# Kernel tuning notes

Measured on AMD Instinct MI355X. Metric: run time of the kernel, lower is better.

The kernel has to match this reference:

```python
import jax, jax.numpy as jnp
import numpy as np

NUM_HEADS = 16

def setup_inputs() -> dict:
    key = jax.random.key(0)
    ks = jax.random.split(key, 7)
    n_node, n_graph, E = 512, 8, 1024
    H = NUM_HEADS
    inp = {
        "query": jax.random.normal(ks[0], (n_node, n_graph, E), jnp.float32),
        "attn_bias": jax.random.normal(ks[1], (n_graph * H, n_node, n_node), jnp.float32),
        "graph_attn_weight": jax.random.normal(ks[2], (n_graph * H, n_node, n_node), jnp.float32),
        "in_w": jax.random.normal(ks[3], (3 * E, E), jnp.float32) * (E ** -0.5),
        "in_b": jnp.zeros((3 * E,), jnp.float32),
        "out_w": jax.random.normal(ks[4], (E, E), jnp.float32) * (E ** -0.5),
        "out_b": jnp.zeros((E,), jnp.float32),
    }
    return inp

def reference(query, attn_bias, graph_attn_weight, in_w, in_b, out_w, out_b):
    n_node, n_graph, E = query.shape
    H = NUM_HEADS
    hd = E // H
    scaling = hd ** -0.5
    # fused QKV projection (torch Linear: x @ W.T + b)
    qkv = query @ in_w.T + in_b                      # [n, g, 3E]
    q, k, v = jnp.split(qkv, 3, axis=-1)             # each [n, g, E]
    def to_heads(x):
        # [n, g, E] -> [g*H, n, hd]
        return x.reshape(n_node, n_graph * H, hd).transpose(1, 0, 2)
    q = to_heads(q) * scaling
    k = to_heads(k)
    v = to_heads(v)
    attn_weights = jnp.einsum('bnd,bmd->bnm', q, k) + attn_bias  # [g*H, n, n]
    attn_probs = jnp.tanh(graph_attn_weight) * jax.nn.softmax(attn_weights, axis=-1)
    attn = jnp.einsum('bnm,bmd->bnd', attn_probs, v)             # [g*H, n, hd]
    attn = attn.transpose(1, 0, 2).reshape(n_node, n_graph, E)
    return attn @ out_w.T + out_b
```

## Files before the change

kernel.cpp:

```cpp
#include <hip/hip_runtime.h>
#include <hip/hip_bf16.h>
#include <cstdint>

#define N_NODE 512
#define N_GRAPH 8
#define EDIM 1024
#define NHEADS 16
#define HD 64
#define GH 128
#define MROWS 4096

typedef short bf16x8 __attribute__((ext_vector_type(8)));
typedef float f32x4  __attribute__((ext_vector_type(4)));

__device__ __forceinline__ short f2bs(float f) {
    union { __hip_bfloat16 h; short s; } u; u.h = __float2bfloat16(f); return u.s;
}
__device__ __forceinline__ float bs2f(short s) {
    union { unsigned u; float f; } v; v.u = ((unsigned)(unsigned short)s) << 16; return v.f;
}
__device__ __forceinline__ float fast_tanh(float x) {
    const float e = __expf(2.f * x);
    return 1.f - __fdividef(2.f, 1.f + e);
}

__device__ __forceinline__ void direct_lds16(const short* g, short* l) {
    __builtin_amdgcn_global_load_lds(
        (const __attribute__((address_space(1))) unsigned int*)(uintptr_t)g,
        (__attribute__((address_space(3))) unsigned int*)(unsigned)(uintptr_t)l,
        16, 0, 0);
}

__global__ __launch_bounds__(256)
void cvt_bf16(const float* __restrict__ in, short* __restrict__ out, int n8)
{
    const int i = blockIdx.x * 256 + threadIdx.x;
    if (i >= n8) return;
    const float4 f0 = *reinterpret_cast<const float4*>(in + (size_t)i * 8);
    const float4 f1 = *reinterpret_cast<const float4*>(in + (size_t)i * 8 + 4);
    bf16x8 h;
    h[0] = f2bs(f0.x); h[1] = f2bs(f0.y); h[2] = f2bs(f0.z); h[3] = f2bs(f0.w);
    h[4] = f2bs(f1.x); h[5] = f2bs(f1.y); h[6] = f2bs(f1.z); h[7] = f2bs(f1.w);
    *reinterpret_cast<bf16x8*>(out + (size_t)i * 8) = h;
}

template<int MODE>
__global__ __launch_bounds__(256)
void gemm_bf16(const short* __restrict__ A, const short* __restrict__ B,
               const float* __restrict__ bias, float* __restrict__ Cout,
               __hip_bfloat16* __restrict__ Cq,
               __hip_bfloat16* __restrict__ Ck,
               __hip_bfloat16* __restrict__ Cv,
               int M, int N, int K)
{
    __shared__ short As[128 * 32];
    __shared__ short Bs[128 * 32];

    const int nwg  = gridDim.x * gridDim.y;
    const int flat = blockIdx.y * gridDim.x + blockIdx.x;
    const int q8   = nwg >> 3;
    const int swz  = (flat & 7) * q8 + (flat >> 3);
    const int bx   = swz % gridDim.x;
    const int by   = swz / gridDim.x;

    const int tid  = threadIdx.x;
    const int m0   = by * 128;
    const int n0   = bx * 128;
    const int lane = tid & 63;
    const int w    = tid >> 6;
    const int l16  = lane & 15;
    const int quad = lane >> 4;
    const int wm   = w & 1;
    const int wn   = w >> 1;
    const int lrow = lane >> 2;
    const int lcol = (lane & 3) << 3;

    const short* ga = A + (size_t)(m0 + w * 16 + lrow) * K + lcol;
    const short* gb = B + (size_t)(n0 + w * 16 + lrow) * K + lcol;
    short* lA = &As[w * 512];
    short* lB = &Bs[w * 512];

    f32x4 acc[4][4];
    #pragma unroll
    for (int mt = 0; mt < 4; mt++)
        #pragma unroll
        for (int nt = 0; nt < 4; nt++)
            acc[mt][nt] = (f32x4){0.f, 0.f, 0.f, 0.f};

    for (int k0 = 0; k0 < K; k0 += 32) {
        direct_lds16(ga + k0, lA);
        direct_lds16(ga + (size_t)64 * K + k0, lA + 2048);
        direct_lds16(gb + k0, lB);
        direct_lds16(gb + (size_t)64 * K + k0, lB + 2048);
        __syncthreads();

        bf16x8 af[4], bfr[4];
        #pragma unroll
        for (int mt = 0; mt < 4; mt++)
            af[mt] = *reinterpret_cast<const bf16x8*>(
                &As[(wm * 64 + mt * 16 + l16) * 32 + quad * 8]);
        #pragma unroll
        for (int nt = 0; nt < 4; nt++)
            bfr[nt] = *reinterpret_cast<const bf16x8*>(
                &Bs[(wn * 64 + nt * 16 + l16) * 32 + quad * 8]);
        #pragma unroll
        for (int mt = 0; mt < 4; mt++)
            #pragma unroll
            for (int nt = 0; nt < 4; nt++)
                acc[mt][nt] = __builtin_amdgcn_mfma_f32_16x16x32_bf16(
                    af[mt], bfr[nt], acc[mt][nt], 0, 0, 0);
        __syncthreads();
    }

    #pragma unroll
    for (int nt = 0; nt < 4; nt++) {
        const int c = n0 + wn * 64 + nt * 16 + l16;
        const float bv = bias[c];
        #pragma unroll
        for (int mt = 0; mt < 4; mt++) {
            #pragma unroll
            for (int rr = 0; rr < 4; rr++) {
                const int r = m0 + wm * 64 + mt * 16 + quad * 4 + rr;
                const float v = acc[mt][nt][rr] + bv;
                if (MODE == 0) {
                    Cout[(size_t)r * N + c] = v;
                } else {
                    const int qsel = c >> 10;
                    const int e = c & 1023;
                    const int head = e >> 6;
                    const int d = e & 63;
                    const int node = r >> 3;
                    const int graph = r & 7;
                    const int b = graph * NHEADS + head;
                    const size_t idx = ((size_t)b * N_NODE + node) * HD + d;
                    if (qsel == 0)      Cq[idx] = __float2bfloat16(v * 0.125f);
                    else if (qsel == 1) Ck[idx] = __float2bfloat16(v);
                    else                Cv[idx] = __float2bfloat16(v);
                }
            }
        }
    }
}

__global__ __launch_bounds__(256)
void transpose_v(const __hip_bfloat16* __restrict__ V,
                 __hip_bfloat16* __restrict__ Vt)
{
    __shared__ short T[64][80];
    const int b = blockIdx.y;
    const int jt = blockIdx.x;
    const int t = threadIdx.x;

    #pragma unroll
    for (int it = 0; it < 2; it++) {
        const int idx = t + it * 256;
        const int j_loc = idx >> 3;
        const int ch = idx & 7;
        bf16x8 v = *reinterpret_cast<const bf16x8*>(
            V + ((size_t)b * N_NODE + jt * 64 + j_loc) * HD + ch * 8);
        *reinterpret_cast<bf16x8*>(&T[j_loc][ch * 8]) = v;
    }
    __syncthreads();
    #pragma unroll
    for (int it = 0; it < 2; it++) {
        const int idx = t + it * 256;
        const int d_loc = idx >> 3;
        const int ch = idx & 7;
        bf16x8 o;
        #pragma unroll
        for (int x = 0; x < 8; x++) o[x] = T[ch * 8 + x][d_loc];
        *reinterpret_cast<bf16x8*>(
            Vt + ((size_t)b * HD + d_loc) * N_NODE + jt * 64 + ch * 8) = o;
    }
}

#define PBS 512

__global__ __launch_bounds__(256, 4)
void attn_mfma(const __hip_bfloat16* __restrict__ Qh,
               const __hip_bfloat16* __restrict__ Kh,
               const __hip_bfloat16* __restrict__ Vt,
               const float* __restrict__ bias,
               const float* __restrict__ gaw,
               __hip_bfloat16* __restrict__ A2)
{
    __shared__ __align__(16) short Pb[16 * PBS];
    __shared__ __align__(16) float mpart[16][4];
    __shared__ __align__(16) float spart[16][4];

    const int b    = blockIdx.y;
    const int i0   = blockIdx.x * 16;
    const int tid  = threadIdx.x;
    const int lane = tid & 63;
    const int w    = tid >> 6;
    const int quad = lane >> 4;
    const int l16  = lane & 15;
    const int row_l = quad * 4;

    f32x4 sreg[8];

    {
        const __hip_bfloat16* Qb =
            Qh + ((size_t)b * N_NODE + i0 + l16) * HD + quad * 8;
        const bf16x8 qa0 = *reinterpret_cast<const bf16x8*>(Qb);
        const bf16x8 qa1 = *reinterpret_cast<const bf16x8*>(Qb + 32);
        const float* bp0 = bias + ((size_t)b * N_NODE + i0 + row_l) * N_NODE + l16;
        float mx[4] = {-1e30f, -1e30f, -1e30f, -1e30f};

        #pragma unroll
        for (int t = 0; t < 8; t++) {
            const int jt = w + 4 * t;
            const __hip_bfloat16* Kb =
                Kh + ((size_t)b * N_NODE + jt * 16 + l16) * HD + quad * 8;
            const bf16x8 k0 = *reinterpret_cast<const bf16x8*>(Kb);
            const bf16x8 k1 = *reinterpret_cast<const bf16x8*>(Kb + 32);
            f32x4 acc = {0.f, 0.f, 0.f, 0.f};
            acc = __builtin_amdgcn_mfma_f32_16x16x32_bf16(qa0, k0, acc, 0, 0, 0);
            acc = __builtin_amdgcn_mfma_f32_16x16x32_bf16(qa1, k1, acc, 0, 0, 0);
            const float* bp = bp0 + jt * 16;
            #pragma unroll
            for (int r = 0; r < 4; r++) {
                acc[r] += bp[(size_t)r * N_NODE];
                mx[r] = fmaxf(mx[r], acc[r]);
            }
            sreg[t] = acc;
        }
        #pragma unroll
        for (int r = 0; r < 4; r++) {
            float m = mx[r];
            m = fmaxf(m, __shfl_xor(m, 1));
            m = fmaxf(m, __shfl_xor(m, 2));
            m = fmaxf(m, __shfl_xor(m, 4));
            m = fmaxf(m, __shfl_xor(m, 8));
            if (l16 == 0) mpart[row_l + r][w] = m;
        }
    }
    __syncthreads();

    {
        float mrow[4];
        #pragma unroll
        for (int r = 0; r < 4; r++) {
            const float4 mp = *reinterpret_cast<const float4*>(mpart[row_l + r]);
            mrow[r] = fmaxf(fmaxf(mp.x, mp.y), fmaxf(mp.z, mp.w));
        }
        float sum[4] = {0.f, 0.f, 0.f, 0.f};
        const float* gp0 = gaw + ((size_t)b * N_NODE + i0 + row_l) * N_NODE + l16;

        #pragma unroll
        for (int t = 0; t < 8; t++) {
            const int jt = w + 4 * t;
            const int colb = (jt * 16 + l16) * 2;
            const float* gp = gp0 + jt * 16;
            #pragma unroll
            for (int r = 0; r < 4; r++) {
                const float e = __expf(sreg[t][r] - mrow[r]);
                sum[r] += e;
                const float g = gp[(size_t)r * N_NODE];
                const float p = fast_tanh(g) * e;
                const int row = row_l + r;
                const int byte = row * (PBS * 2) + (colb ^ ((row & 7) << 4));
                *reinterpret_cast<short*>(reinterpret_cast<char*>(Pb) + byte) = f2bs(p);
            }
        }
        #pragma unroll
        for (int r = 0; r < 4; r++) {
            float s = sum[r];
            s += __shfl_xor(s, 1);
            s += __shfl_xor(s, 2);
            s += __shfl_xor(s, 4);
            s += __shfl_xor(s, 8);
            if (l16 == 0) spart[row_l + r][w] = s;
        }
    }
    __syncthreads();

    {
        const __hip_bfloat16* Vb =
            Vt + ((size_t)b * HD + w * 16 + l16) * N_NODE + quad * 8;
        f32x4 acc = {0.f, 0.f, 0.f, 0.f};
        #pragma unroll
        for (int j32 = 0; j32 < 16; j32++) {
            const int byte = l16 * (PBS * 2)
                           + ((j32 * 64 + quad * 16) ^ ((l16 & 7) << 4));
            const bf16x8 af = *reinterpret_cast<const bf16x8*>(
                reinterpret_cast<const char*>(Pb) + byte);
            const bf16x8 bfr = *reinterpret_cast<const bf16x8*>(Vb + j32 * 32);
            acc = __builtin_amdgcn_mfma_f32_16x16x32_bf16(af, bfr, acc, 0, 0, 0);
        }
        const int node0 = i0 + quad * 4;
        __hip_bfloat16* op = A2 + (size_t)node0 * (N_GRAPH * EDIM)
                           + (b >> 4) * EDIM + (b & 15) * HD + w * 16 + l16;
        #pragma unroll
        for (int r = 0; r < 4; r++) {
            const float4 sp = *reinterpret_cast<const float4*>(spart[quad * 4 + r]);
            const float rs = 1.f / (sp.x + sp.y + sp.z + sp.w);
            op[(size_t)r * (N_GRAPH * EDIM)] = __float2bfloat16(acc[r] * rs);
        }
    }
}

extern "C" void kernel_launch(void* const* d_in, const int* in_sizes, int n_in,
                              void* d_out, int out_size, void* d_ws, size_t ws_size,
                              hipStream_t stream) {
    const float* query     = (const float*)d_in[0];
    const float* attn_bias = (const float*)d_in[1];
    const float* gaw       = (const float*)d_in[2];
    const float* in_w      = (const float*)d_in[3];
    const float* in_b      = (const float*)d_in[4];
    const float* out_w     = (const float*)d_in[5];
    const float* out_b     = (const float*)d_in[6];
    float* out = (float*)d_out;

    short* wsp = (short*)d_ws;
    const size_t hsz = (size_t)GH * N_NODE * HD;
    short* Q   = wsp;
    short* K   = wsp + hsz;
    short* V   = wsp + 2 * hsz;
    short* Vt  = wsp + 3 * hsz;
    short* A2  = V;
    short* qb  = Vt;
    short* wbi = wsp + 4 * hsz;
    short* wbo = wbi + (size_t)3 * EDIM * EDIM;

    cvt_bf16<<<dim3(MROWS * EDIM / 2048), 256, 0, stream>>>(query, qb, MROWS * EDIM / 8);
    cvt_bf16<<<dim3(3 * EDIM * EDIM / 2048), 256, 0, stream>>>(in_w, wbi, 3 * EDIM * EDIM / 8);
    cvt_bf16<<<dim3(EDIM * EDIM / 2048), 256, 0, stream>>>(out_w, wbo, EDIM * EDIM / 8);

    gemm_bf16<1><<<dim3(24, 32), 256, 0, stream>>>(
        qb, wbi, in_b, nullptr,
        (__hip_bfloat16*)Q, (__hip_bfloat16*)K, (__hip_bfloat16*)V,
        MROWS, 3 * EDIM, EDIM);

    transpose_v<<<dim3(8, GH), 256, 0, stream>>>(
        (const __hip_bfloat16*)V, (__hip_bfloat16*)Vt);

    attn_mfma<<<dim3(N_NODE / 16, GH), 256, 0, stream>>>(
        (const __hip_bfloat16*)Q, (const __hip_bfloat16*)K,
        (const __hip_bfloat16*)Vt, attn_bias, gaw, (__hip_bfloat16*)A2);

    gemm_bf16<0><<<dim3(8, 32), 256, 0, stream>>>(
        (const short*)A2, wbo, out_b, out,
        nullptr, nullptr, nullptr, MROWS, EDIM, EDIM);
}
```

Baseline: 426.7 us.

## Pipeline GEMM loads with triple buffering and restructure attention for vectorized loads

The GEMM now uses a three-stage LDS ring with direct global-to-LDS loads issued one tile ahead and explicit vmcnt waits, replacing the two-barrier-per-iteration loop. It gains a BN template so the output projection uses 64-wide tiles and a larger grid. The attention kernel swaps the MFMA operand order so each lane owns one row, which allows float4 loads of bias and graph weights. It also prefetches K and V fragments into registers, swizzles the block order, and lowers launch bounds to 3 waves per SIMD. The trade is higher register and LDS pressure, and less occupancy, in return for overlapping memory with compute and coalescing the reads.

```diff
diff --git a/kernel.cpp b/kernel.cpp
--- a/kernel.cpp
+++ b/kernel.cpp
@@ -15,9 +15,6 @@
 
 __device__ __forceinline__ short f2bs(float f) {
     union { __hip_bfloat16 h; short s; } u; u.h = __float2bfloat16(f); return u.s;
-}
-__device__ __forceinline__ float bs2f(short s) {
-    union { unsigned u; float f; } v; v.u = ((unsigned)(unsigned short)s) << 16; return v.f;
 }
 __device__ __forceinline__ float fast_tanh(float x) {
     const float e = __expf(2.f * x);
@@ -44,7 +41,7 @@
     *reinterpret_cast<bf16x8*>(out + (size_t)i * 8) = h;
 }
 
-template<int MODE>
+template<int MODE, int BN>
 __global__ __launch_bounds__(256)
 void gemm_bf16(const short* __restrict__ A, const short* __restrict__ B,
                const float* __restrict__ bias, float* __restrict__ Cout,
@@ -53,8 +50,8 @@
                __hip_bfloat16* __restrict__ Cv,
                int M, int N, int K)
 {
-    __shared__ short As[128 * 32];
-    __shared__ short Bs[128 * 32];
+    __shared__ short As[3][128 * 32];
+    __shared__ short Bs[3][BN * 32];
 
     const int nwg  = gridDim.x * gridDim.y;
     const int flat = blockIdx.y * gridDim.x + blockIdx.x;
@@ -65,7 +62,7 @@
 
     const int tid  = threadIdx.x;
     const int m0   = by * 128;
-    const int n0   = bx * 128;
+    const int n0   = bx * BN;
     const int lane = tid & 63;
     const int w    = tid >> 6;
     const int l16  = lane & 15;
@@ -77,44 +74,65 @@
 
     const short* ga = A + (size_t)(m0 + w * 16 + lrow) * K + lcol;
     const short* gb = B + (size_t)(n0 + w * 16 + lrow) * K + lcol;
-    short* lA = &As[w * 512];
-    short* lB = &Bs[w * 512];
-
-    f32x4 acc[4][4];
+
+    constexpr int NTC = BN / 32;
+
+    f32x4 acc[4][NTC];
     #pragma unroll
     for (int mt = 0; mt < 4; mt++)
         #pragma unroll
-        for (int nt = 0; nt < 4; nt++)
+        for (int nt = 0; nt < NTC; nt++)
             acc[mt][nt] = (f32x4){0.f, 0.f, 0.f, 0.f};
 
-    for (int k0 = 0; k0 < K; k0 += 32) {
-        direct_lds16(ga + k0, lA);
-        direct_lds16(ga + (size_t)64 * K + k0, lA + 2048);
-        direct_lds16(gb + k0, lB);
-        direct_lds16(gb + (size_t)64 * K + k0, lB + 2048);
-        __syncthreads();
-
-        bf16x8 af[4], bfr[4];
+    auto STAGE = [&](int kk, int buf) {
+        short* lA = &As[buf][w * 512];
+        direct_lds16(ga + kk, lA);
+        direct_lds16(ga + (size_t)64 * K + kk, lA + 2048);
+        short* lB = &Bs[buf][w * 512];
+        direct_lds16(gb + kk, lB);
+        if constexpr (BN == 128)
+            direct_lds16(gb + (size_t)64 * K + kk, lB + 2048);
+    };
+
+    const int NT = K >> 5;
+    STAGE(0, 0);
+    int cur = 0, nxt = 1;
+    for (int t = 0; t < NT; ++t) {
+        if (t + 1 < NT) {
+            STAGE((t + 1) << 5, nxt);
+            if constexpr (BN == 128)
+                asm volatile("s_waitcnt vmcnt(4)" ::: "memory");
+            else
+                asm volatile("s_waitcnt vmcnt(3)" ::: "memory");
+        } else {
+            asm volatile("s_waitcnt vmcnt(0)" ::: "memory");
+        }
+        __builtin_amdgcn_s_barrier();
+        __builtin_amdgcn_sched_barrier(0);
+
+        bf16x8 af[4], bfr[NTC];
         #pragma unroll
         for (int mt = 0; mt < 4; mt++)
             af[mt] = *reinterpret_cast<const bf16x8*>(
-                &As[(wm * 64 + mt * 16 + l16) * 32 + quad * 8]);
-        #pragma unroll
-        for (int nt = 0; nt < 4; nt++)
+                &As[cur][(wm * 64 + mt * 16 + l16) * 32 + quad * 8]);
+        #pragma unroll
+        for (int nt = 0; nt < NTC; nt++)
             bfr[nt] = *reinterpret_cast<const bf16x8*>(
-                &Bs[(wn * 64 + nt * 16 + l16) * 32 + quad * 8]);
+                &Bs[cur][(wn * (BN / 2) + nt * 16 + l16) * 32 + quad * 8]);
         #pragma unroll
         for (int mt = 0; mt < 4; mt++)
             #pragma unroll
-            for (int nt = 0; nt < 4; nt++)
+            for (int nt = 0; nt < NTC; nt++)
                 acc[mt][nt] = __builtin_amdgcn_mfma_f32_16x16x32_bf16(
                     af[mt], bfr[nt], acc[mt][nt], 0, 0, 0);
-        __syncthreads();
-    }
-
-    #pragma unroll
-    for (int nt = 0; nt < 4; nt++) {
-        const int c = n0 + wn * 64 + nt * 16 + l16;
+
+        cur = (cur == 2) ? 0 : cur + 1;
+        nxt = (nxt == 2) ? 0 : nxt + 1;
+    }
+
+    #pragma unroll
+    for (int nt = 0; nt < NTC; nt++) {
+        const int c = n0 + wn * (BN / 2) + nt * 16 + l16;
         const float bv = bias[c];
         #pragma unroll
         for (int mt = 0; mt < 4; mt++) {
@@ -174,9 +192,7 @@
     }
 }
 
-#define PBS 512
-
-__global__ __launch_bounds__(256, 4)
+__global__ __launch_bounds__(256, 3)
 void attn_mfma(const __hip_bfloat16* __restrict__ Qh,
                const __hip_bfloat16* __restrict__ Kh,
                const __hip_bfloat16* __restrict__ Vt,
@@ -184,109 +200,109 @@
                const float* __restrict__ gaw,
                __hip_bfloat16* __restrict__ A2)
 {
-    __shared__ __align__(16) short Pb[16 * PBS];
+    __shared__ __align__(16) short Pb[16 * 512];
     __shared__ __align__(16) float mpart[16][4];
     __shared__ __align__(16) float spart[16][4];
 
-    const int b    = blockIdx.y;
-    const int i0   = blockIdx.x * 16;
+    const int flat = blockIdx.y * gridDim.x + blockIdx.x;
+    const int swz  = (flat & 7) * 512 + (flat >> 3);
+    const int b    = swz >> 5;
+    const int i0   = (swz & 31) * 16;
+
     const int tid  = threadIdx.x;
     const int lane = tid & 63;
     const int w    = tid >> 6;
     const int quad = lane >> 4;
     const int l16  = lane & 15;
-    const int row_l = quad * 4;
+
+    const bf16x8* Qb = reinterpret_cast<const bf16x8*>(
+        Qh + ((size_t)b * N_NODE + i0 + l16) * HD + quad * 8);
+    const bf16x8 qa0 = Qb[0];
+    const bf16x8 qa1 = Qb[4];
+
+    bf16x8 kf[8][2];
+    #pragma unroll
+    for (int t = 0; t < 8; ++t) {
+        const int jt = w + 4 * t;
+        const bf16x8* Kb = reinterpret_cast<const bf16x8*>(
+            Kh + ((size_t)b * N_NODE + jt * 16 + l16) * HD + quad * 8);
+        kf[t][0] = Kb[0];
+        kf[t][1] = Kb[4];
+    }
+    const float* bp0 = bias + ((size_t)b * N_NODE + i0 + l16) * N_NODE
+                     + w * 16 + quad * 4;
+    f32x4 breg[8];
+    #pragma unroll
+    for (int t = 0; t < 8; ++t)
+        breg[t] = *reinterpret_cast<const f32x4*>(bp0 + t * 64);
 
     f32x4 sreg[8];
+    float mx = -1e30f;
+    #pragma unroll
+    for (int t = 0; t < 8; ++t) {
+        f32x4 acc = {0.f, 0.f, 0.f, 0.f};
+        acc = __builtin_amdgcn_mfma_f32_16x16x32_bf16(kf[t][0], qa0, acc, 0, 0, 0);
+        acc = __builtin_amdgcn_mfma_f32_16x16x32_bf16(kf[t][1], qa1, acc, 0, 0, 0);
+        acc += breg[t];
+        sreg[t] = acc;
+        mx = fmaxf(mx, fmaxf(fmaxf(acc[0], acc[1]), fmaxf(acc[2], acc[3])));
+    }
+
+    const float* gp0 = gaw + ((size_t)b * N_NODE + i0 + l16) * N_NODE
+                     + w * 16 + quad * 4;
+    f32x4 greg[8];
+    #pragma unroll
+    for (int t = 0; t < 8; ++t)
+        greg[t] = *reinterpret_cast<const f32x4*>(gp0 + t * 64);
+
+    mx = fmaxf(mx, __shfl_xor(mx, 16));
+    mx = fmaxf(mx, __shfl_xor(mx, 32));
+    if (lane < 16) mpart[l16][w] = mx;
+    __syncthreads();
+
+    const float4 mp4 = *reinterpret_cast<const float4*>(mpart[l16]);
+    const float m = fmaxf(fmaxf(mp4.x, mp4.y), fmaxf(mp4.z, mp4.w));
+
+    const bf16x8* Vb = reinterpret_cast<const bf16x8*>(
+        Vt + ((size_t)b * HD + w * 16 + l16) * N_NODE + quad * 8);
+    bf16x8 vf[16];
+    #pragma unroll
+    for (int j32 = 0; j32 < 16; ++j32)
+        vf[j32] = Vb[j32 * 4];
+
+    float sum = 0.f;
+    #pragma unroll
+    for (int t = 0; t < 8; ++t) {
+        const int jt = w + 4 * t;
+        short4 p4;
+        {
+            const float e0 = __expf(sreg[t][0] - m);
+            const float e1 = __expf(sreg[t][1] - m);
+            const float e2 = __expf(sreg[t][2] - m);
+            const float e3 = __expf(sreg[t][3] - m);
+            sum += (e0 + e1) + (e2 + e3);
+            p4.x = f2bs(fast_tanh(greg[t][0]) * e0);
+            p4.y = f2bs(fast_tanh(greg[t][1]) * e1);
+            p4.z = f2bs(fast_tanh(greg[t][2]) * e2);
+            p4.w = f2bs(fast_tanh(greg[t][3]) * e3);
+        }
+        const int byte = l16 * 1024 + ((jt * 32 + quad * 8) ^ ((l16 & 7) << 4));
+        *reinterpret_cast<short4*>(reinterpret_cast<char*>(Pb) + byte) = p4;
+    }
+    sum += __shfl_xor(sum, 16);
+    sum += __shfl_xor(sum, 32);
+    if (lane < 16) spart[l16][w] = sum;
+    __syncthreads();
 
     {
-        const __hip_bfloat16* Qb =
-            Qh + ((size_t)b * N_NODE + i0 + l16) * HD + quad * 8;
-        const bf16x8 qa0 = *reinterpret_cast<const bf16x8*>(Qb);
-        const bf16x8 qa1 = *reinterpret_cast<const bf16x8*>(Qb + 32);
-        const float* bp0 = bias + ((size_t)b * N_NODE + i0 + row_l) * N_NODE + l16;
-        float mx[4] = {-1e30f, -1e30f, -1e30f, -1e30f};
-
-        #pragma unroll
-        for (int t = 0; t < 8; t++) {
-            const int jt = w + 4 * t;
-            const __hip_bfloat16* Kb =
-                Kh + ((size_t)b * N_NODE + jt * 16 + l16) * HD + quad * 8;
-            const bf16x8 k0 = *reinterpret_cast<const bf16x8*>(Kb);
-            const bf16x8 k1 = *reinterpret_cast<const bf16x8*>(Kb + 32);
-            f32x4 acc = {0.f, 0.f, 0.f, 0.f};
-            acc = __builtin_amdgcn_mfma_f32_16x16x32_bf16(qa0, k0, acc, 0, 0, 0);
-            acc = __builtin_amdgcn_mfma_f32_16x16x32_bf16(qa1, k1, acc, 0, 0, 0);
-            const float* bp = bp0 + jt * 16;
-            #pragma unroll
-            for (int r = 0; r < 4; r++) {
-                acc[r] += bp[(size_t)r * N_NODE];
-                mx[r] = fmaxf(mx[r], acc[r]);
-            }
-            sreg[t] = acc;
-        }
-        #pragma unroll
-        for (int r = 0; r < 4; r++) {
-            float m = mx[r];
-            m = fmaxf(m, __shfl_xor(m, 1));
-            m = fmaxf(m, __shfl_xor(m, 2));
-            m = fmaxf(m, __shfl_xor(m, 4));
-            m = fmaxf(m, __shfl_xor(m, 8));
-            if (l16 == 0) mpart[row_l + r][w] = m;
-        }
-    }
-    __syncthreads();
-
-    {
-        float mrow[4];
-        #pragma unroll
-        for (int r = 0; r < 4; r++) {
-            const float4 mp = *reinterpret_cast<const float4*>(mpart[row_l + r]);
-            mrow[r] = fmaxf(fmaxf(mp.x, mp.y), fmaxf(mp.z, mp.w));
-        }
-        float sum[4] = {0.f, 0.f, 0.f, 0.f};
-        const float* gp0 = gaw + ((size_t)b * N_NODE + i0 + row_l) * N_NODE + l16;
-
-        #pragma unroll
-        for (int t = 0; t < 8; t++) {
-            const int jt = w + 4 * t;
-            const int colb = (jt * 16 + l16) * 2;
-            const float* gp = gp0 + jt * 16;
-            #pragma unroll
-            for (int r = 0; r < 4; r++) {
-                const float e = __expf(sreg[t][r] - mrow[r]);
-                sum[r] += e;
-                const float g = gp[(size_t)r * N_NODE];
-                const float p = fast_tanh(g) * e;
-                const int row = row_l + r;
-                const int byte = row * (PBS * 2) + (colb ^ ((row & 7) << 4));
-                *reinterpret_cast<short*>(reinterpret_cast<char*>(Pb) + byte) = f2bs(p);
-            }
-        }
-        #pragma unroll
-        for (int r = 0; r < 4; r++) {
-            float s = sum[r];
-            s += __shfl_xor(s, 1);
-            s += __shfl_xor(s, 2);
-            s += __shfl_xor(s, 4);
-            s += __shfl_xor(s, 8);
-            if (l16 == 0) spart[row_l + r][w] = s;
-        }
-    }
-    __syncthreads();
-
-    {
-        const __hip_bfloat16* Vb =
-            Vt + ((size_t)b * HD + w * 16 + l16) * N_NODE + quad * 8;
         f32x4 acc = {0.f, 0.f, 0.f, 0.f};
         #pragma unroll
-        for (int j32 = 0; j32 < 16; j32++) {
-            const int byte = l16 * (PBS * 2)
+        for (int j32 = 0; j32 < 16; ++j32) {
+            const int byte = l16 * 1024
                            + ((j32 * 64 + quad * 16) ^ ((l16 & 7) << 4));
             const bf16x8 af = *reinterpret_cast<const bf16x8*>(
                 reinterpret_cast<const char*>(Pb) + byte);
-            const bf16x8 bfr = *reinterpret_cast<const bf16x8*>(Vb + j32 * 32);
-            acc = __builtin_amdgcn_mfma_f32_16x16x32_bf16(af, bfr, acc, 0, 0, 0);
+            acc = __builtin_amdgcn_mfma_f32_16x16x32_bf16(af, vf[j32], acc, 0, 0, 0);
         }
         const int node0 = i0 + quad * 4;
         __hip_bfloat16* op = A2 + (size_t)node0 * (N_GRAPH * EDIM)
@@ -327,7 +343,7 @@
     cvt_bf16<<<dim3(3 * EDIM * EDIM / 2048), 256, 0, stream>>>(in_w, wbi, 3 * EDIM * EDIM / 8);
     cvt_bf16<<<dim3(EDIM * EDIM / 2048), 256, 0, stream>>>(out_w, wbo, EDIM * EDIM / 8);
 
-    gemm_bf16<1><<<dim3(24, 32), 256, 0, stream>>>(
+    gemm_bf16<1, 128><<<dim3(24, 32), 256, 0, stream>>>(
         qb, wbi, in_b, nullptr,
         (__hip_bfloat16*)Q, (__hip_bfloat16*)K, (__hip_bfloat16*)V,
         MROWS, 3 * EDIM, EDIM);
@@ -339,7 +355,7 @@
         (const __hip_bfloat16*)Q, (const __hip_bfloat16*)K,
         (const __hip_bfloat16*)Vt, attn_bias, gaw, (__hip_bfloat16*)A2);
 
-    gemm_bf16<0><<<dim3(8, 32), 256, 0, stream>>>(
+    gemm_bf16<0, 64><<<dim3(16, 32), 256, 0, stream>>>(
         (const short*)A2, wbo, out_b, out,
         nullptr, nullptr, nullptr, MROWS, EDIM, EDIM);
 }
```

New measurement: 411.4 us. 1.04x faster.
